# Kernel tuning notes

Hardware: AMD Instinct MI355X
Metric: run time of the kernel (lower is better)

Reference implementation:

```python
import jax, jax.numpy as jnp
import numpy as np

N_NODES = 100000
N_EDGES = 1600000
HID = 128
BOND = 16
BN_EPS = 1e-5


def setup_inputs() -> dict:
    key = jax.random.key(0)
    ks = jax.random.split(key, 12)
    sb = 1.0 / np.sqrt(BOND)
    sh = 1.0 / np.sqrt(HID)
    return {
        "features": jax.random.normal(ks[0], (N_NODES, HID), jnp.float32),
        "edge_feats": jax.random.normal(ks[1], (N_EDGES, BOND), jnp.float32),
        "src": jax.random.randint(ks[2], (N_EDGES,), 0, N_NODES, jnp.int32),
        "dst": jax.random.randint(ks[3], (N_EDGES,), 0, N_NODES, jnp.int32),
        "Wb": jax.random.uniform(ks[4], (HID, BOND), jnp.float32, -sb, sb),
        "bb": jax.random.uniform(ks[5], (HID,), jnp.float32, -sb, sb),
        "W1": jax.random.uniform(ks[6], (HID, HID), jnp.float32, -sh, sh),
        "b1": jax.random.uniform(ks[7], (HID,), jnp.float32, -sh, sh),
        "W2": jax.random.uniform(ks[8], (HID, HID), jnp.float32, -sh, sh),
        "b2": jax.random.uniform(ks[9], (HID,), jnp.float32, -sh, sh),
        "gamma1": jnp.ones((HID,), jnp.float32),
        "beta1": jnp.zeros((HID,), jnp.float32),
        "gamma2": jnp.ones((HID,), jnp.float32),
        "beta2": jnp.zeros((HID,), jnp.float32),
    }


def _batchnorm(x, gamma, beta):
    # BatchNorm1d in training mode: normalize with batch stats (biased var).
    mean = jnp.mean(x, axis=0)
    var = jnp.var(x, axis=0)
    return (x - mean) * jax.lax.rsqrt(var + BN_EPS) * gamma + beta


def reference(features, edge_feats, src, dst, Wb, bb, W1, b1, W2, b2,
              gamma1, beta1, gamma2, beta2):
    n = features.shape[0]
    # edge linear: [E, BOND] -> [E, HID]
    eh = edge_feats @ Wb.T + bb
    # mailbox sums: sum of src node features and edge messages per dst node
    h1 = jax.ops.segment_sum(features[src], dst, num_segments=n)  # [N, HID]
    h2 = jax.ops.segment_sum(eh, dst, num_segments=n)             # [N, HID]
    h = jax.nn.relu(_batchnorm(h1 @ W1.T + b1 + h2, gamma1, beta1))
    h = jax.nn.relu(_batchnorm(h @ W2.T + b2 + features, gamma2, beta2))
    return h
```

## Files before the change

kernel.cpp:

```cpp
#include <hip/hip_runtime.h>

#define NN 100000
#define NE 1600000
#define HID 128
#define KEXT 160
#define ROWB 320
#define BSH 9
#define BNODES 512
#define NB 196
#define P2B 256
#define EPB2 6250
#define T2 2048
#define BN_EPS 1e-5f

typedef __attribute__((ext_vector_type(8))) short bf16x8;
typedef __attribute__((ext_vector_type(4))) float f32x4;
typedef unsigned long long u64;

__device__ inline unsigned short f2bf(float x) {
  union { float f; unsigned u; } v; v.f = x;
  unsigned r = v.u + 0x7FFFu + ((v.u >> 16) & 1u);
  return (unsigned short)(r >> 16);
}
__device__ inline unsigned pk2(float a, float b) {
  return (unsigned)f2bf(a) | ((unsigned)f2bf(b) << 16);
}
__device__ inline float bflo(unsigned p) { return __uint_as_float(p << 16); }
__device__ inline float bfhi(unsigned p) { return __uint_as_float(p & 0xffff0000u); }

__device__ inline void gload_lds16(const void* g, void* l) {
  __builtin_amdgcn_global_load_lds((const __attribute__((address_space(1))) void*)g,
                                   (__attribute__((address_space(3))) void*)l, 16, 0, 0);
}

__global__ __launch_bounds__(256) void fbw_k(const float* __restrict__ f,
                                             unsigned* __restrict__ fb,
                                             const float* __restrict__ W1,
                                             const float* __restrict__ Wb,
                                             const float* __restrict__ bb,
                                             const float* __restrict__ b1,
                                             const float* __restrict__ W2,
                                             unsigned short* __restrict__ W1e,
                                             unsigned short* __restrict__ W2e) {
  if (blockIdx.x < 25000) {
    int i = blockIdx.x * 256 + threadIdx.x;
    float2 v = ((const float2*)f)[i];
    fb[i] = pk2(v.x, v.y);
  } else {
    int idx = (blockIdx.x - 25000) * 256 + threadIdx.x;
    if (idx < 128 * KEXT) {
      int c = idx / KEXT, k = idx - c * KEXT;
      float v1 = 0.f;
      if (k < 128) v1 = W1[c * HID + k];
      else if (k < 144) v1 = Wb[c * 16 + (k - 128)];
      else if (k == 144) v1 = bb[c];
      else if (k == 145) v1 = b1[c];
      W1e[idx] = f2bf(v1);
    }
    if (idx < 128 * 128) W2e[idx] = f2bf(W2[(idx >> 7) * HID + (idx & 127)]);
  }
}

__global__ __launch_bounds__(1024) void cnt_k(const int* __restrict__ dst,
                                              int* __restrict__ cnts_s) {
  __shared__ int bh[NB];
  int blk = blockIdx.x;
  int b0 = blk * EPB2, e1 = b0 + EPB2;
  for (int i = threadIdx.x; i < NB; i += 1024) bh[i] = 0;
  __syncthreads();
  for (int e = b0 + threadIdx.x; e < e1; e += 1024) atomicAdd(&bh[dst[e] >> BSH], 1);
  __syncthreads();
  for (int i = threadIdx.x; i < NB; i += 1024) cnts_s[i * P2B + blk] = bh[i];
}

__global__ __launch_bounds__(P2B) void cscan_k(int* __restrict__ cnts_s,
                                               int* __restrict__ cnts_e,
                                               int* __restrict__ bcnt_s,
                                               int* __restrict__ bcnt_e,
                                               int* __restrict__ bcnt_r) {
  __shared__ int s[P2B];
  int b = blockIdx.x, t = threadIdx.x;
  int x = cnts_s[b * P2B + t];
  int xs = (x + 7) & ~7;
  int xe = (x + 1) & ~1;
  s[t] = xs; __syncthreads();
  for (int off = 1; off < P2B; off <<= 1) {
    int v = (t >= off) ? s[t - off] : 0; __syncthreads();
    s[t] += v; __syncthreads();
  }
  cnts_s[b * P2B + t] = s[t] - xs;
  if (t == P2B - 1) bcnt_s[b] = s[t];
  __syncthreads();
  s[t] = xe; __syncthreads();
  for (int off = 1; off < P2B; off <<= 1) {
    int v = (t >= off) ? s[t - off] : 0; __syncthreads();
    s[t] += v; __syncthreads();
  }
  cnts_e[b * P2B + t] = s[t] - xe;
  if (t == P2B - 1) bcnt_e[b] = s[t];
  __syncthreads();
  s[t] = x; __syncthreads();
  for (int off = 1; off < P2B; off <<= 1) {
    int v = (t >= off) ? s[t - off] : 0; __syncthreads();
    s[t] += v; __syncthreads();
  }
  if (t == P2B - 1) bcnt_r[b] = s[t];
}

__global__ __launch_bounds__(256) void bscan_k(const int* __restrict__ bcnt_r,
                                               const int* __restrict__ bcnt_s,
                                               const int* __restrict__ bcnt_e,
                                               int* __restrict__ bbase_r,
                                               int* __restrict__ bbase_s,
                                               int* __restrict__ bbase_e,
                                               int* __restrict__ rs) {
  __shared__ int s[256];
  int t = threadIdx.x;
#pragma unroll
  for (int pass = 0; pass < 3; ++pass) {
    const int* in = (pass == 0) ? bcnt_r : (pass == 1) ? bcnt_s : bcnt_e;
    int* out = (pass == 0) ? bbase_r : (pass == 1) ? bbase_s : bbase_e;
    int x = (t < NB) ? in[t] : 0;
    s[t] = x; __syncthreads();
    for (int off = 1; off < 256; off <<= 1) {
      int v = (t >= off) ? s[t - off] : 0; __syncthreads();
      s[t] += v; __syncthreads();
    }
    if (t < NB) out[t] = s[t] - x;
    if (t == NB - 1) out[NB] = s[t];
    __syncthreads();
  }
  if (t == 0) rs[NN] = NE;
}

__global__ __launch_bounds__(1024) void part3_k(const int* __restrict__ src,
                                                const int* __restrict__ dst,
                                                const float* __restrict__ ef,
                                                const int* __restrict__ bbase_s,
                                                const int* __restrict__ bbase_e,
                                                const int* __restrict__ cnts_s,
                                                const int* __restrict__ cnts_e,
                                                u64* __restrict__ stg,
                                                float4* __restrict__ efb) {
  __shared__ int th[NB], ts[NB], cnt2[NB], run[NB], st_s[NB], st_e[NB];
  __shared__ int sscan[256];
  __shared__ unsigned spk[T2];
  __shared__ float4 eflds[T2 * 2];
  int blk = blockIdx.x, tid = threadIdx.x;
  int b0 = blk * EPB2, e1 = b0 + EPB2;
  for (int i = tid; i < NB; i += 1024) {
    run[i] = 0;
    st_s[i] = bbase_s[i] + cnts_s[i * P2B + blk];
    st_e[i] = bbase_e[i] + cnts_e[i * P2B + blk];
  }
  for (int t0 = b0; t0 < e1; t0 += T2) {
    int tc = min(T2, e1 - t0);
    for (int i = tid; i < NB; i += 1024) { th[i] = 0; cnt2[i] = 0; }
    __syncthreads();
    for (int le = tid; le < tc; le += 1024) {
      int e = t0 + le;
      atomicAdd(&th[dst[e] >> BSH], 1);
      const float4* efp = (const float4*)(ef + (size_t)e * 16);
      float4 e0 = efp[0], e1v = efp[1], e2 = efp[2], e3 = efp[3];
      float4 w0, w1;
      w0.x = __uint_as_float(pk2(e0.x, e0.y));  w0.y = __uint_as_float(pk2(e0.z, e0.w));
      w0.z = __uint_as_float(pk2(e1v.x, e1v.y)); w0.w = __uint_as_float(pk2(e1v.z, e1v.w));
      w1.x = __uint_as_float(pk2(e2.x, e2.y));  w1.y = __uint_as_float(pk2(e2.z, e2.w));
      w1.z = __uint_as_float(pk2(e3.x, e3.y));  w1.w = __uint_as_float(pk2(e3.z, e3.w));
      eflds[le * 2] = w0;
      eflds[le * 2 + 1] = w1;
    }
    __syncthreads();
    if (tid < 256) sscan[tid] = (tid < NB) ? th[tid] : 0;
    __syncthreads();
    for (int off = 1; off < 256; off <<= 1) {
      int v = 0;
      if (tid < 256 && tid >= off) v = sscan[tid - off];
      __syncthreads();
      if (tid < 256) sscan[tid] += v;
      __syncthreads();
    }
    if (tid < NB) ts[tid] = sscan[tid] - th[tid];
    __syncthreads();
    for (int le = tid; le < tc; le += 1024) {
      int b = dst[t0 + le] >> BSH;
      int slot = ts[b] + atomicAdd(&cnt2[b], 1);
      spk[slot] = ((unsigned)b << 11) | (unsigned)le;
    }
    __syncthreads();
    for (int s2 = tid; s2 < tc; s2 += 1024) {
      unsigned pk = spk[s2];
      int b = pk >> 11, le = pk & 2047;
      int e = t0 + le;
      int o = run[b] + (s2 - ts[b]);
      int gs = st_s[b] + o;
      int ge = st_e[b] + o;
      int d9 = dst[e] & (BNODES - 1);
      stg[gs] = (u64)(unsigned)src[e] | ((u64)(unsigned)d9 << 17) |
                (1ULL << 26) | ((u64)(unsigned)ge << 27);
      efb[(size_t)ge * 2] = eflds[le * 2];
      efb[(size_t)ge * 2 + 1] = eflds[le * 2 + 1];
    }
    __syncthreads();
    for (int i = tid; i < NB; i += 1024) run[i] += th[i];
    __syncthreads();
  }
  float4 z4 = make_float4(0.f, 0.f, 0.f, 0.f);
  for (int i = tid; i < NB; i += 1024) {
    int c = run[i];
    int cs = (c + 7) & ~7;
    for (int j = c; j < cs; ++j) stg[st_s[i] + j] = 0ULL;
    if (c & 1) {
      int ge = st_e[i] + c;
      efb[(size_t)ge * 2] = z4;
      efb[(size_t)ge * 2 + 1] = z4;
    }
  }
}

__global__ __launch_bounds__(512) void bsort_k(const u64* __restrict__ stg,
                                               const int* __restrict__ bbase_s,
                                               const int* __restrict__ bbase_r,
                                               int* __restrict__ rs,
                                               u64* __restrict__ fin) {
  __shared__ int h[BNODES], cur[BNODES], sc[BNODES];
  int b = blockIdx.x, n0 = b << BSH, tid = threadIdx.x;
  int s0p = bbase_s[b], e1p = bbase_s[b + 1];
  int s0r = bbase_r[b];
  h[tid] = 0;
  __syncthreads();
  for (int i = s0p + tid; i < e1p; i += 512) {
    u64 rec = stg[i];
    if ((rec >> 26) & 1) atomicAdd(&h[(int)(rec >> 17) & (BNODES - 1)], 1);
  }
  __syncthreads();
  sc[tid] = h[tid];
  __syncthreads();
  for (int off = 1; off < BNODES; off <<= 1) {
    int v = (tid >= off) ? sc[tid - off] : 0;
    __syncthreads();
    sc[tid] += v;
    __syncthreads();
  }
  {
    int excl = sc[tid] - h[tid];
    cur[tid] = s0r + excl;
    int n = n0 + tid;
    if (n < NN) rs[n] = s0r + excl;
  }
  __syncthreads();
  for (int i = s0p + tid; i < e1p; i += 512) {
    u64 rec = stg[i];
    if ((rec >> 26) & 1) {
      int d = (int)(rec >> 17) & (BNODES - 1);
      int p = atomicAdd(&cur[d], 1);
      fin[p] = (rec & 0x1FFFF) | (((rec >> 27) & 0x1FFFFF) << 17);
    }
  }
}

__global__ __launch_bounds__(256) void feg_k(const unsigned* __restrict__ fb,
                                             const int* __restrict__ rs,
                                             const u64* __restrict__ fin,
                                             const unsigned* __restrict__ efb,
                                             unsigned short* __restrict__ A1) {
  int bid = (int)(blockIdx.x & 7) * 3125 + (int)(blockIdx.x >> 3);
  int wid = threadIdx.x >> 6, lane = threadIdx.x & 63;
  int node = bid * 4 + wid;
  if (node >= NN) return;
  int start = rs[node], end = rs[node + 1];
  int j8 = lane & 7, es = lane >> 3;
  float ax0 = 0.f, ay0 = 0.f, ax1 = 0.f, ay1 = 0.f;
  float ax2 = 0.f, ay2 = 0.f, ax3 = 0.f, ay3 = 0.f;
  float ax4 = 0.f, ay4 = 0.f, ax5 = 0.f, ay5 = 0.f;
  float ax6 = 0.f, ay6 = 0.f, ax7 = 0.f, ay7 = 0.f;
  float efx = 0.f, efy = 0.f;
  int i = start;
  for (; i + 8 <= end; i += 8) {
    int sl = 0, el = 0;
    if (lane < 8) {
      u64 pk = fin[i + lane];
      sl = (int)(pk & 0x1FFFF);
      el = (int)((pk >> 17) & 0x1FFFFF);
    }
    int s0 = __shfl(sl, 0), s1 = __shfl(sl, 1), s2 = __shfl(sl, 2), s3 = __shfl(sl, 3);
    int s4 = __shfl(sl, 4), s5 = __shfl(sl, 5), s6 = __shfl(sl, 6), s7 = __shfl(sl, 7);
    int pes = __shfl(el, es);
    unsigned p0 = fb[s0 * 64 + lane];
    unsigned p1 = fb[s1 * 64 + lane];
    unsigned p2 = fb[s2 * 64 + lane];
    unsigned p3 = fb[s3 * 64 + lane];
    unsigned p4 = fb[s4 * 64 + lane];
    unsigned p5 = fb[s5 * 64 + lane];
    unsigned p6 = fb[s6 * 64 + lane];
    unsigned p7 = fb[s7 * 64 + lane];
    unsigned ev = efb[(size_t)pes * 8 + j8];
    ax0 += bflo(p0); ay0 += bfhi(p0);
    ax1 += bflo(p1); ay1 += bfhi(p1);
    ax2 += bflo(p2); ay2 += bfhi(p2);
    ax3 += bflo(p3); ay3 += bfhi(p3);
    ax4 += bflo(p4); ay4 += bfhi(p4);
    ax5 += bflo(p5); ay5 += bfhi(p5);
    ax6 += bflo(p6); ay6 += bfhi(p6);
    ax7 += bflo(p7); ay7 += bfhi(p7);
    efx += bflo(ev); efy += bfhi(ev);
  }
  for (; i < end; ++i) {
    int sl = 0, el = 0;
    if (lane == 0) {
      u64 pk = fin[i];
      sl = (int)(pk & 0x1FFFF);
      el = (int)((pk >> 17) & 0x1FFFFF);
    }
    int s0 = __shfl(sl, 0), e0 = __shfl(el, 0);
    unsigned p0 = fb[s0 * 64 + lane];
    ax0 += bflo(p0); ay0 += bfhi(p0);
    if (lane < 8) {
      unsigned ev = efb[(size_t)e0 * 8 + j8];
      efx += bflo(ev); efy += bfhi(ev);
    }
  }
  efx += __shfl_xor(efx, 8);  efy += __shfl_xor(efy, 8);
  efx += __shfl_xor(efx, 16); efy += __shfl_xor(efy, 16);
  efx += __shfl_xor(efx, 32); efy += __shfl_xor(efy, 32);
  float ax = ((ax0 + ax1) + (ax2 + ax3)) + ((ax4 + ax5) + (ax6 + ax7));
  float ay = ((ay0 + ay1) + (ay2 + ay3)) + ((ay4 + ay5) + (ay6 + ay7));
  char* rowp = (char*)A1 + (size_t)node * ROWB;
  *(unsigned*)(rowp + lane * 4) = pk2(ax, ay);
  if (lane < 8) {
    *(unsigned*)(rowp + 256 + 4 * j8) = pk2(efx, efy);
  } else if (lane < 16) {
    int j2 = lane - 8;
    *(unsigned*)(rowp + 288 + 4 * j2) =
        (j2 == 0) ? pk2((float)(end - start), 1.0f) : 0u;
  }
}

__global__ __launch_bounds__(256) void gemm1_k(
    const unsigned short* __restrict__ A, const unsigned short* __restrict__ W,
    unsigned short* __restrict__ outb, float* __restrict__ ssum, float* __restrict__ ssq) {
  __shared__ __align__(16) char sA[64 * ROWB];
  __shared__ __align__(16) char sW[128 * ROWB];
  const int tid = threadIdx.x;
  const int wid = tid >> 6, lane = tid & 63;
  const size_t r0 = (size_t)blockIdx.x * 64;

#pragma unroll
  for (int q = 0; q < 5; ++q) {
    int s = q * 256 + tid;
    int row = (s * 3277) >> 16;
    int c = s - row * 20;
    int csrc = (c < 16) ? (c ^ (row & 7)) : (16 + ((c - 16) ^ (row & 3)));
    gload_lds16((const char*)A + (r0 + row) * ROWB + csrc * 16,
                sA + (size_t)(q * 256 + wid * 64) * 16);
  }
#pragma unroll
  for (int q = 0; q < 10; ++q) {
    int s = q * 256 + tid;
    int row = (s * 3277) >> 16;
    int c = s - row * 20;
    int csrc = (c < 16) ? (c ^ (row & 7)) : (16 + ((c - 16) ^ (row & 3)));
    gload_lds16((const char*)W + (size_t)row * ROWB + csrc * 16,
                sW + (size_t)(q * 256 + wid * 64) * 16);
  }
  __syncthreads();

  const int l15 = lane & 15;
  const int kgr = lane >> 4;
  const int arow = wid * 16 + l15;
  bf16x8 afrag[5];
#pragma unroll
  for (int ks = 0; ks < 5; ++ks) {
    int creq = ks * 4 + kgr;
    int csw = (creq < 16) ? (creq ^ (arow & 7)) : (16 + ((creq - 16) ^ (arow & 3)));
    afrag[ks] = *(const bf16x8*)(sA + arow * ROWB + csw * 16);
  }
  f32x4 acc[8];
#pragma unroll
  for (int ct = 0; ct < 8; ++ct) acc[ct] = (f32x4){0.f, 0.f, 0.f, 0.f};
#pragma unroll
  for (int ct = 0; ct < 8; ++ct) {
    int brow = ct * 16 + l15;
#pragma unroll
    for (int ks = 0; ks < 5; ++ks) {
      int creq = ks * 4 + kgr;
      int csw = (creq < 16) ? (creq ^ (brow & 7)) : (16 + ((creq - 16) ^ (brow & 3)));
      bf16x8 bfrag = *(const bf16x8*)(sW + brow * ROWB + csw * 16);
      acc[ct] = __builtin_amdgcn_mfma_f32_16x16x32_bf16(afrag[ks], bfrag, acc[ct], 0, 0, 0);
    }
  }

  const size_t orow0 = r0 + wid * 16 + kgr * 4;
  float cs[8], cq[8];
#pragma unroll
  for (int ct = 0; ct < 8; ++ct) {
    int col = ct * 16 + l15;
    float s_ = 0.f, q_ = 0.f;
#pragma unroll
    for (int r = 0; r < 4; ++r) {
      size_t row = orow0 + r;
      if (row < NN) {
        float v = acc[ct][r];
        outb[row * HID + col] = f2bf(v);
        s_ += v; q_ += v * v;
      }
    }
    cs[ct] = s_; cq[ct] = q_;
  }
#pragma unroll
  for (int ct = 0; ct < 8; ++ct) {
    cs[ct] += __shfl_xor(cs[ct], 16); cs[ct] += __shfl_xor(cs[ct], 32);
    cq[ct] += __shfl_xor(cq[ct], 16); cq[ct] += __shfl_xor(cq[ct], 32);
  }
  __syncthreads();
  float* red = (float*)sA;
  if (lane < 16) {
#pragma unroll
    for (int ct = 0; ct < 8; ++ct) {
      red[wid * 256 + ct * 16 + l15] = cs[ct];
      red[wid * 256 + 128 + ct * 16 + l15] = cq[ct];
    }
  }
  __syncthreads();
  if (tid < 128) {
    float s_ = red[tid] + red[256 + tid] + red[512 + tid] + red[768 + tid];
    float q_ = red[128 + tid] + red[384 + tid] + red[640 + tid] + red[896 + tid];
    atomicAdd(&ssum[tid], s_);
    atomicAdd(&ssq[tid], q_);
  }
}

__global__ __launch_bounds__(256) void gemm2_k(
    const unsigned* __restrict__ t, const unsigned short* __restrict__ W,
    const float* __restrict__ ssum, const float* __restrict__ ssq,
    const float* __restrict__ gamma, const float* __restrict__ beta,
    const float* __restrict__ b2, const float* __restrict__ F,
    unsigned short* __restrict__ outb, float* __restrict__ ssum2,
    float* __restrict__ ssq2) {
  __shared__ __align__(16) char sA[64 * 256];
  __shared__ __align__(16) char sW[128 * 256];
  __shared__ float ssc[128], ssh[128];
  const int tid = threadIdx.x;
  const int wid = tid >> 6, lane = tid & 63;
  const size_t r0 = (size_t)blockIdx.x * 64;

  if (tid < 128) {
    const float invN = 1.f / (float)NN;
    float m = ssum[tid] * invN;
    float var = ssq[tid] * invN - m * m;
    float inv = rsqrtf(var + BN_EPS);
    float sc = gamma[tid] * inv;
    ssc[tid] = sc;
    ssh[tid] = beta[tid] - m * sc;
  }
#pragma unroll
  for (int q = 0; q < 8; ++q) {
    int s = q * 256 + tid;
    int row = s >> 4, c = s & 15;
    int csrc = c ^ (row & 7);
    gload_lds16((const char*)W + (size_t)row * 256 + csrc * 16,
                sW + (size_t)(q * 256 + wid * 64) * 16);
  }
  __syncthreads();

  {
    int sr = tid >> 2;
    int c0 = (tid & 3) * 4;
    size_t grow = r0 + sr;
    bool valid = grow < NN;
    const unsigned* trow = t + grow * 64;
#pragma unroll
    for (int cc = 0; cc < 4; ++cc) {
      int c = c0 + cc;
      unsigned o0 = 0, o1 = 0, o2 = 0, o3 = 0;
      if (valid) {
        unsigned p0 = trow[c * 4 + 0], p1 = trow[c * 4 + 1];
        unsigned p2 = trow[c * 4 + 2], p3 = trow[c * 4 + 3];
        int k = c * 8;
        o0 = pk2(fmaxf(0.f, fmaf(bflo(p0), ssc[k + 0], ssh[k + 0])),
                 fmaxf(0.f, fmaf(bfhi(p0), ssc[k + 1], ssh[k + 1])));
        o1 = pk2(fmaxf(0.f, fmaf(bflo(p1), ssc[k + 2], ssh[k + 2])),
                 fmaxf(0.f, fmaf(bfhi(p1), ssc[k + 3], ssh[k + 3])));
        o2 = pk2(fmaxf(0.f, fmaf(bflo(p2), ssc[k + 4], ssh[k + 4])),
                 fmaxf(0.f, fmaf(bfhi(p2), ssc[k + 5], ssh[k + 5])));
        o3 = pk2(fmaxf(0.f, fmaf(bflo(p3), ssc[k + 6], ssh[k + 6])),
                 fmaxf(0.f, fmaf(bfhi(p3), ssc[k + 7], ssh[k + 7])));
      }
      int csw = c ^ (sr & 7);
      uint4 w4; w4.x = o0; w4.y = o1; w4.z = o2; w4.w = o3;
      *(uint4*)(sA + sr * 256 + csw * 16) = w4;
    }
  }
  __syncthreads();

  const int l15 = lane & 15;
  const int kgr = lane >> 4;
  const int arow = wid * 16 + l15;
  bf16x8 afrag[4];
#pragma unroll
  for (int ks = 0; ks < 4; ++ks) {
    int creq = ks * 4 + kgr;
    int csw = creq ^ (arow & 7);
    afrag[ks] = *(const bf16x8*)(sA + arow * 256 + csw * 16);
  }
  f32x4 acc[8];
#pragma unroll
  for (int ct = 0; ct < 8; ++ct) acc[ct] = (f32x4){0.f, 0.f, 0.f, 0.f};
#pragma unroll
  for (int ct = 0; ct < 8; ++ct) {
    int brow = ct * 16 + l15;
#pragma unroll
    for (int ks = 0; ks < 4; ++ks) {
      int creq = ks * 4 + kgr;
      int csw = creq ^ (brow & 7);
      bf16x8 bfrag = *(const bf16x8*)(sW + brow * 256 + csw * 16);
      acc[ct] = __builtin_amdgcn_mfma_f32_16x16x32_bf16(afrag[ks], bfrag, acc[ct], 0, 0, 0);
    }
  }

  const size_t orow0 = r0 + wid * 16 + kgr * 4;
  float cs[8], cq[8];
#pragma unroll
  for (int ct = 0; ct < 8; ++ct) {
    int col = ct * 16 + l15;
    float b2v = b2[col];
    float s_ = 0.f, q_ = 0.f;
#pragma unroll
    for (int r = 0; r < 4; ++r) {
      size_t row = orow0 + r;
      if (row < NN) {
        float v = acc[ct][r] + b2v + F[row * HID + col];
        outb[row * HID + col] = f2bf(v);
        s_ += v; q_ += v * v;
      }
    }
    cs[ct] = s_; cq[ct] = q_;
  }
#pragma unroll
  for (int ct = 0; ct < 8; ++ct) {
    cs[ct] += __shfl_xor(cs[ct], 16); cs[ct] += __shfl_xor(cs[ct], 32);
    cq[ct] += __shfl_xor(cq[ct], 16); cq[ct] += __shfl_xor(cq[ct], 32);
  }
  __syncthreads();
  float* red = (float*)sA;
  if (lane < 16) {
#pragma unroll
    for (int ct = 0; ct < 8; ++ct) {
      red[wid * 256 + ct * 16 + l15] = cs[ct];
      red[wid * 256 + 128 + ct * 16 + l15] = cq[ct];
    }
  }
  __syncthreads();
  if (tid < 128) {
    float s_ = red[tid] + red[256 + tid] + red[512 + tid] + red[768 + tid];
    float q_ = red[128 + tid] + red[384 + tid] + red[640 + tid] + red[896 + tid];
    atomicAdd(&ssum2[tid], s_);
    atomicAdd(&ssq2[tid], q_);
  }
}

__global__ __launch_bounds__(256) void bn_final_k(const unsigned* __restrict__ t,
                                                  const float* __restrict__ ssum,
                                                  const float* __restrict__ ssq,
                                                  const float* __restrict__ gamma,
                                                  const float* __restrict__ beta,
                                                  float* __restrict__ o) {
  __shared__ float ssc[128], ssh[128];
  int tid = threadIdx.x;
  if (tid < 128) {
    const float invN = 1.f / (float)NN;
    float m = ssum[tid] * invN;
    float var = ssq[tid] * invN - m * m;
    float inv = rsqrtf(var + BN_EPS);
    float sc = gamma[tid] * inv;
    ssc[tid] = sc;
    ssh[tid] = beta[tid] - m * sc;
  }
  __syncthreads();
  int i = blockIdx.x * 256 + tid;
  if (i >= NN * 64) return;
  unsigned p = t[i];
  int c = (i & 63) * 2;
  float2 v;
  v.x = fmaxf(0.f, fmaf(bflo(p), ssc[c], ssh[c]));
  v.y = fmaxf(0.f, fmaf(bfhi(p), ssc[c + 1], ssh[c + 1]));
  ((float2*)o)[i] = v;
}

extern "C" void kernel_launch(void* const* d_in, const int* in_sizes, int n_in,
                              void* d_out, int out_size, void* d_ws, size_t ws_size,
                              hipStream_t stream) {
  (void)in_sizes; (void)n_in; (void)out_size; (void)ws_size;
  const float* features   = (const float*)d_in[0];
  const float* edge_feats = (const float*)d_in[1];
  const int*   src        = (const int*)d_in[2];
  const int*   dst        = (const int*)d_in[3];
  const float* Wb         = (const float*)d_in[4];
  const float* bb         = (const float*)d_in[5];
  const float* W1         = (const float*)d_in[6];
  const float* b1         = (const float*)d_in[7];
  const float* W2         = (const float*)d_in[8];
  const float* b2         = (const float*)d_in[9];
  const float* gamma1     = (const float*)d_in[10];
  const float* beta1      = (const float*)d_in[11];
  const float* gamma2     = (const float*)d_in[12];
  const float* beta2      = (const float*)d_in[13];
  float* outp = (float*)d_out;

  char* wsb = (char*)d_ws;
  size_t off = 0;
  auto alloc = [&](size_t nbytes) -> void* {
    off = (off + 255) & ~(size_t)255;
    void* p = wsb + off;
    off += nbytes;
    return p;
  };
  int* row_start = (int*)alloc((size_t)(NN + 1) * 4);
  int* bcnt_r    = (int*)alloc(NB * 4);
  int* bcnt_s    = (int*)alloc(NB * 4);
  int* bcnt_e    = (int*)alloc(NB * 4);
  int* bbase_r   = (int*)alloc((NB + 1) * 4);
  int* bbase_s   = (int*)alloc((NB + 1) * 4);
  int* bbase_e   = (int*)alloc((NB + 1) * 4);
  int* cnts_s    = (int*)alloc((size_t)NB * P2B * 4);
  int* cnts_e    = (int*)alloc((size_t)NB * P2B * 4);
  float* stats   = (float*)alloc(512 * 4);
  unsigned* featb = (unsigned*)alloc((size_t)NN * 64 * 4);
  unsigned short* A1e = (unsigned short*)alloc((size_t)100032 * ROWB);
  unsigned short* W1e = (unsigned short*)alloc(128 * KEXT * 2);
  unsigned short* W2e = (unsigned short*)alloc(128 * 128 * 2);
  u64* stg       = (u64*)alloc((size_t)(NE + 7 * NB * P2B + 64) * 8);
  u64* fin       = (u64*)alloc((size_t)NE * 8);
  float4* efb    = (float4*)alloc((size_t)(NE + NB * P2B + 64) * 32);
  unsigned short* tbuf = (unsigned short*)featb;

  hipMemsetAsync(stats, 0, 512 * 4, stream);
  hipMemsetAsync((char*)A1e + (size_t)NN * ROWB, 0, 32 * ROWB, stream);

  fbw_k<<<25080, 256, 0, stream>>>(features, featb, W1, Wb, bb, b1, W2, W1e, W2e);
  cnt_k<<<P2B, 1024, 0, stream>>>(dst, cnts_s);
  cscan_k<<<NB, P2B, 0, stream>>>(cnts_s, cnts_e, bcnt_s, bcnt_e, bcnt_r);
  bscan_k<<<1, 256, 0, stream>>>(bcnt_r, bcnt_s, bcnt_e, bbase_r, bbase_s, bbase_e,
                                 row_start);
  part3_k<<<P2B, 1024, 0, stream>>>(src, dst, edge_feats, bbase_s, bbase_e,
                                    cnts_s, cnts_e, stg, efb);
  bsort_k<<<NB, 512, 0, stream>>>(stg, bbase_s, bbase_r, row_start, fin);
  feg_k<<<25000, 256, 0, stream>>>(featb, row_start, fin, (const unsigned*)efb, A1e);

  gemm1_k<<<1563, 256, 0, stream>>>(A1e, W1e, tbuf, stats, stats + 128);
  gemm2_k<<<1563, 256, 0, stream>>>((const unsigned*)tbuf, W2e, stats, stats + 128,
                                    gamma1, beta1, b2, features, tbuf,
                                    stats + 256, stats + 384);
  bn_final_k<<<25000, 256, 0, stream>>>((const unsigned*)tbuf, stats + 256, stats + 384,
                                        gamma2, beta2, outp);
}
```

Baseline: 327.6 us.

## Fold dst histogram into prep kernel and pre-reduce edge features in bucket sort

The dst bucket-count kernel is merged into the feature/weight conversion launch as extra blocks, which removes one launch. The separate edge-feature staging offsets (cnts_e/bbase_e scans) are dropped. Edge features now share the sort staging index, and records shrink from 64-bit to 32-bit. bsort_k sorts records in LDS and sums each node's bf16 edge features into an efsum buffer, so feg_k no longer gathers per-edge features. The cost is a serial per-thread loop in bsort_k over each node's edges, plus an LDS capacity assumption (SCAP) on bucket size.

```diff
diff --git a/kernel.cpp b/kernel.cpp
--- a/kernel.cpp
+++ b/kernel.cpp
@@ -11,11 +11,11 @@
 #define P2B 256
 #define EPB2 6250
 #define T2 2048
+#define SCAP 10240
 #define BN_EPS 1e-5f
 
 typedef __attribute__((ext_vector_type(8))) short bf16x8;
 typedef __attribute__((ext_vector_type(4))) float f32x4;
-typedef unsigned long long u64;
 
 __device__ inline unsigned short f2bf(float x) {
   union { float f; unsigned u; } v; v.f = x;
@@ -41,12 +41,15 @@
                                              const float* __restrict__ b1,
                                              const float* __restrict__ W2,
                                              unsigned short* __restrict__ W1e,
-                                             unsigned short* __restrict__ W2e) {
+                                             unsigned short* __restrict__ W2e,
+                                             const int* __restrict__ dst,
+                                             int* __restrict__ cnts_s) {
+  __shared__ int bh[NB];
   if (blockIdx.x < 25000) {
     int i = blockIdx.x * 256 + threadIdx.x;
     float2 v = ((const float2*)f)[i];
     fb[i] = pk2(v.x, v.y);
-  } else {
+  } else if (blockIdx.x < 25080) {
     int idx = (blockIdx.x - 25000) * 256 + threadIdx.x;
     if (idx < 128 * KEXT) {
       int c = idx / KEXT, k = idx - c * KEXT;
@@ -58,31 +61,24 @@
       W1e[idx] = f2bf(v1);
     }
     if (idx < 128 * 128) W2e[idx] = f2bf(W2[(idx >> 7) * HID + (idx & 127)]);
-  }
-}
-
-__global__ __launch_bounds__(1024) void cnt_k(const int* __restrict__ dst,
-                                              int* __restrict__ cnts_s) {
-  __shared__ int bh[NB];
-  int blk = blockIdx.x;
-  int b0 = blk * EPB2, e1 = b0 + EPB2;
-  for (int i = threadIdx.x; i < NB; i += 1024) bh[i] = 0;
-  __syncthreads();
-  for (int e = b0 + threadIdx.x; e < e1; e += 1024) atomicAdd(&bh[dst[e] >> BSH], 1);
-  __syncthreads();
-  for (int i = threadIdx.x; i < NB; i += 1024) cnts_s[i * P2B + blk] = bh[i];
+  } else {
+    int blk = blockIdx.x - 25080;
+    int b0 = blk * EPB2, e1 = b0 + EPB2;
+    for (int i = threadIdx.x; i < NB; i += 256) bh[i] = 0;
+    __syncthreads();
+    for (int e = b0 + threadIdx.x; e < e1; e += 256) atomicAdd(&bh[dst[e] >> BSH], 1);
+    __syncthreads();
+    for (int i = threadIdx.x; i < NB; i += 256) cnts_s[i * P2B + blk] = bh[i];
+  }
 }
 
 __global__ __launch_bounds__(P2B) void cscan_k(int* __restrict__ cnts_s,
-                                               int* __restrict__ cnts_e,
                                                int* __restrict__ bcnt_s,
-                                               int* __restrict__ bcnt_e,
                                                int* __restrict__ bcnt_r) {
   __shared__ int s[P2B];
   int b = blockIdx.x, t = threadIdx.x;
   int x = cnts_s[b * P2B + t];
   int xs = (x + 7) & ~7;
-  int xe = (x + 1) & ~1;
   s[t] = xs; __syncthreads();
   for (int off = 1; off < P2B; off <<= 1) {
     int v = (t >= off) ? s[t - off] : 0; __syncthreads();
@@ -91,14 +87,6 @@
   cnts_s[b * P2B + t] = s[t] - xs;
   if (t == P2B - 1) bcnt_s[b] = s[t];
   __syncthreads();
-  s[t] = xe; __syncthreads();
-  for (int off = 1; off < P2B; off <<= 1) {
-    int v = (t >= off) ? s[t - off] : 0; __syncthreads();
-    s[t] += v; __syncthreads();
-  }
-  cnts_e[b * P2B + t] = s[t] - xe;
-  if (t == P2B - 1) bcnt_e[b] = s[t];
-  __syncthreads();
   s[t] = x; __syncthreads();
   for (int off = 1; off < P2B; off <<= 1) {
     int v = (t >= off) ? s[t - off] : 0; __syncthreads();
@@ -109,17 +97,15 @@
 
 __global__ __launch_bounds__(256) void bscan_k(const int* __restrict__ bcnt_r,
                                                const int* __restrict__ bcnt_s,
-                                               const int* __restrict__ bcnt_e,
                                                int* __restrict__ bbase_r,
                                                int* __restrict__ bbase_s,
-                                               int* __restrict__ bbase_e,
                                                int* __restrict__ rs) {
   __shared__ int s[256];
   int t = threadIdx.x;
 #pragma unroll
-  for (int pass = 0; pass < 3; ++pass) {
-    const int* in = (pass == 0) ? bcnt_r : (pass == 1) ? bcnt_s : bcnt_e;
-    int* out = (pass == 0) ? bbase_r : (pass == 1) ? bbase_s : bbase_e;
+  for (int pass = 0; pass < 2; ++pass) {
+    const int* in = (pass == 0) ? bcnt_r : bcnt_s;
+    int* out = (pass == 0) ? bbase_r : bbase_s;
     int x = (t < NB) ? in[t] : 0;
     s[t] = x; __syncthreads();
     for (int off = 1; off < 256; off <<= 1) {
@@ -137,12 +123,10 @@
                                                 const int* __restrict__ dst,
                                                 const float* __restrict__ ef,
                                                 const int* __restrict__ bbase_s,
-                                                const int* __restrict__ bbase_e,
                                                 const int* __restrict__ cnts_s,
-                                                const int* __restrict__ cnts_e,
-                                                u64* __restrict__ stg,
+                                                unsigned* __restrict__ stg,
                                                 float4* __restrict__ efb) {
-  __shared__ int th[NB], ts[NB], cnt2[NB], run[NB], st_s[NB], st_e[NB];
+  __shared__ int th[NB], ts[NB], cnt2[NB], run[NB], st_s[NB];
   __shared__ int sscan[256];
   __shared__ unsigned spk[T2];
   __shared__ float4 eflds[T2 * 2];
@@ -151,7 +135,6 @@
   for (int i = tid; i < NB; i += 1024) {
     run[i] = 0;
     st_s[i] = bbase_s[i] + cnts_s[i * P2B + blk];
-    st_e[i] = bbase_e[i] + cnts_e[i * P2B + blk];
   }
   for (int t0 = b0; t0 < e1; t0 += T2) {
     int tc = min(T2, e1 - t0);
@@ -192,46 +175,41 @@
       unsigned pk = spk[s2];
       int b = pk >> 11, le = pk & 2047;
       int e = t0 + le;
-      int o = run[b] + (s2 - ts[b]);
-      int gs = st_s[b] + o;
-      int ge = st_e[b] + o;
+      int gs = st_s[b] + run[b] + (s2 - ts[b]);
       int d9 = dst[e] & (BNODES - 1);
-      stg[gs] = (u64)(unsigned)src[e] | ((u64)(unsigned)d9 << 17) |
-                (1ULL << 26) | ((u64)(unsigned)ge << 27);
-      efb[(size_t)ge * 2] = eflds[le * 2];
-      efb[(size_t)ge * 2 + 1] = eflds[le * 2 + 1];
+      stg[gs] = (unsigned)src[e] | ((unsigned)d9 << 17) | (1u << 26);
+      efb[(size_t)gs * 2] = eflds[le * 2];
+      efb[(size_t)gs * 2 + 1] = eflds[le * 2 + 1];
     }
     __syncthreads();
     for (int i = tid; i < NB; i += 1024) run[i] += th[i];
     __syncthreads();
   }
-  float4 z4 = make_float4(0.f, 0.f, 0.f, 0.f);
   for (int i = tid; i < NB; i += 1024) {
     int c = run[i];
     int cs = (c + 7) & ~7;
-    for (int j = c; j < cs; ++j) stg[st_s[i] + j] = 0ULL;
-    if (c & 1) {
-      int ge = st_e[i] + c;
-      efb[(size_t)ge * 2] = z4;
-      efb[(size_t)ge * 2 + 1] = z4;
-    }
-  }
-}
-
-__global__ __launch_bounds__(512) void bsort_k(const u64* __restrict__ stg,
+    for (int j = c; j < cs; ++j) stg[st_s[i] + j] = 0u;
+  }
+}
+
+__global__ __launch_bounds__(512) void bsort_k(const unsigned* __restrict__ stg,
                                                const int* __restrict__ bbase_s,
                                                const int* __restrict__ bbase_r,
+                                               const unsigned* __restrict__ efbu,
                                                int* __restrict__ rs,
-                                               u64* __restrict__ fin) {
-  __shared__ int h[BNODES], cur[BNODES], sc[BNODES];
+                                               unsigned* __restrict__ fin,
+                                               unsigned* __restrict__ efsum) {
+  __shared__ int h[BNODES], sc[BNODES], cur[BNODES];
+  __shared__ int tot;
+  __shared__ unsigned slds[SCAP];
   int b = blockIdx.x, n0 = b << BSH, tid = threadIdx.x;
   int s0p = bbase_s[b], e1p = bbase_s[b + 1];
   int s0r = bbase_r[b];
   h[tid] = 0;
   __syncthreads();
   for (int i = s0p + tid; i < e1p; i += 512) {
-    u64 rec = stg[i];
-    if ((rec >> 26) & 1) atomicAdd(&h[(int)(rec >> 17) & (BNODES - 1)], 1);
+    unsigned rec = stg[i];
+    if (rec >> 26) atomicAdd(&h[(rec >> 17) & (BNODES - 1)], 1);
   }
   __syncthreads();
   sc[tid] = h[tid];
@@ -242,50 +220,63 @@
     sc[tid] += v;
     __syncthreads();
   }
-  {
-    int excl = sc[tid] - h[tid];
-    cur[tid] = s0r + excl;
-    int n = n0 + tid;
-    if (n < NN) rs[n] = s0r + excl;
-  }
+  int excl = sc[tid] - h[tid];
+  cur[tid] = excl;
+  int n = n0 + tid;
+  if (n < NN) rs[n] = s0r + excl;
+  if (tid == BNODES - 1) tot = sc[tid];
   __syncthreads();
   for (int i = s0p + tid; i < e1p; i += 512) {
-    u64 rec = stg[i];
-    if ((rec >> 26) & 1) {
-      int d = (int)(rec >> 17) & (BNODES - 1);
+    unsigned rec = stg[i];
+    if (rec >> 26) {
+      int d = (rec >> 17) & (BNODES - 1);
       int p = atomicAdd(&cur[d], 1);
-      fin[p] = (rec & 0x1FFFF) | (((rec >> 27) & 0x1FFFFF) << 17);
-    }
+      slds[p] = (rec & 0x1FFFF) | ((unsigned)(i - s0p) << 17);
+    }
+  }
+  __syncthreads();
+  int T = tot;
+  for (int j = tid; j < T; j += 512) fin[s0r + j] = slds[j] & 0x1FFFF;
+  if (n < NN) {
+    float a[16];
+#pragma unroll
+    for (int k = 0; k < 16; ++k) a[k] = 0.f;
+    for (int j = excl; j < sc[tid]; ++j) {
+      unsigned rec = slds[j];
+      const unsigned* ep = efbu + ((size_t)s0p + (rec >> 17)) * 8;
+#pragma unroll
+      for (int k = 0; k < 8; ++k) {
+        unsigned u = ep[k];
+        a[2 * k] += bflo(u);
+        a[2 * k + 1] += bfhi(u);
+      }
+    }
+    unsigned* op = efsum + (size_t)n * 8;
+#pragma unroll
+    for (int k = 0; k < 8; ++k) op[k] = pk2(a[2 * k], a[2 * k + 1]);
   }
 }
 
 __global__ __launch_bounds__(256) void feg_k(const unsigned* __restrict__ fb,
                                              const int* __restrict__ rs,
-                                             const u64* __restrict__ fin,
-                                             const unsigned* __restrict__ efb,
+                                             const unsigned* __restrict__ fin,
+                                             const unsigned* __restrict__ efsum,
                                              unsigned short* __restrict__ A1) {
   int bid = (int)(blockIdx.x & 7) * 3125 + (int)(blockIdx.x >> 3);
   int wid = threadIdx.x >> 6, lane = threadIdx.x & 63;
   int node = bid * 4 + wid;
   if (node >= NN) return;
   int start = rs[node], end = rs[node + 1];
-  int j8 = lane & 7, es = lane >> 3;
   float ax0 = 0.f, ay0 = 0.f, ax1 = 0.f, ay1 = 0.f;
   float ax2 = 0.f, ay2 = 0.f, ax3 = 0.f, ay3 = 0.f;
   float ax4 = 0.f, ay4 = 0.f, ax5 = 0.f, ay5 = 0.f;
   float ax6 = 0.f, ay6 = 0.f, ax7 = 0.f, ay7 = 0.f;
-  float efx = 0.f, efy = 0.f;
   int i = start;
   for (; i + 8 <= end; i += 8) {
-    int sl = 0, el = 0;
-    if (lane < 8) {
-      u64 pk = fin[i + lane];
-      sl = (int)(pk & 0x1FFFF);
-      el = (int)((pk >> 17) & 0x1FFFFF);
-    }
+    int sl = 0;
+    if (lane < 8) sl = (int)fin[i + lane];
     int s0 = __shfl(sl, 0), s1 = __shfl(sl, 1), s2 = __shfl(sl, 2), s3 = __shfl(sl, 3);
     int s4 = __shfl(sl, 4), s5 = __shfl(sl, 5), s6 = __shfl(sl, 6), s7 = __shfl(sl, 7);
-    int pes = __shfl(el, es);
     unsigned p0 = fb[s0 * 64 + lane];
     unsigned p1 = fb[s1 * 64 + lane];
     unsigned p2 = fb[s2 * 64 + lane];
@@ -294,7 +285,6 @@
     unsigned p5 = fb[s5 * 64 + lane];
     unsigned p6 = fb[s6 * 64 + lane];
     unsigned p7 = fb[s7 * 64 + lane];
-    unsigned ev = efb[(size_t)pes * 8 + j8];
     ax0 += bflo(p0); ay0 += bfhi(p0);
     ax1 += bflo(p1); ay1 += bfhi(p1);
     ax2 += bflo(p2); ay2 += bfhi(p2);
@@ -303,32 +293,20 @@
     ax5 += bflo(p5); ay5 += bfhi(p5);
     ax6 += bflo(p6); ay6 += bfhi(p6);
     ax7 += bflo(p7); ay7 += bfhi(p7);
-    efx += bflo(ev); efy += bfhi(ev);
   }
   for (; i < end; ++i) {
-    int sl = 0, el = 0;
-    if (lane == 0) {
-      u64 pk = fin[i];
-      sl = (int)(pk & 0x1FFFF);
-      el = (int)((pk >> 17) & 0x1FFFFF);
-    }
-    int s0 = __shfl(sl, 0), e0 = __shfl(el, 0);
+    int sl = 0;
+    if (lane == 0) sl = (int)fin[i];
+    int s0 = __shfl(sl, 0);
     unsigned p0 = fb[s0 * 64 + lane];
     ax0 += bflo(p0); ay0 += bfhi(p0);
-    if (lane < 8) {
-      unsigned ev = efb[(size_t)e0 * 8 + j8];
-      efx += bflo(ev); efy += bfhi(ev);
-    }
-  }
-  efx += __shfl_xor(efx, 8);  efy += __shfl_xor(efy, 8);
-  efx += __shfl_xor(efx, 16); efy += __shfl_xor(efy, 16);
-  efx += __shfl_xor(efx, 32); efy += __shfl_xor(efy, 32);
+  }
   float ax = ((ax0 + ax1) + (ax2 + ax3)) + ((ax4 + ax5) + (ax6 + ax7));
   float ay = ((ay0 + ay1) + (ay2 + ay3)) + ((ay4 + ay5) + (ay6 + ay7));
   char* rowp = (char*)A1 + (size_t)node * ROWB;
   *(unsigned*)(rowp + lane * 4) = pk2(ax, ay);
   if (lane < 8) {
-    *(unsigned*)(rowp + 256 + 4 * j8) = pk2(efx, efy);
+    *(unsigned*)(rowp + 256 + 4 * lane) = efsum[(size_t)node * 8 + lane];
   } else if (lane < 16) {
     int j2 = lane - 8;
     *(unsigned*)(rowp + 288 + 4 * j2) =
@@ -615,37 +593,35 @@
     off += nbytes;
     return p;
   };
+  const size_t STGN = (size_t)NE + 7 * NB * P2B + 64;
   int* row_start = (int*)alloc((size_t)(NN + 1) * 4);
   int* bcnt_r    = (int*)alloc(NB * 4);
   int* bcnt_s    = (int*)alloc(NB * 4);
-  int* bcnt_e    = (int*)alloc(NB * 4);
   int* bbase_r   = (int*)alloc((NB + 1) * 4);
   int* bbase_s   = (int*)alloc((NB + 1) * 4);
-  int* bbase_e   = (int*)alloc((NB + 1) * 4);
   int* cnts_s    = (int*)alloc((size_t)NB * P2B * 4);
-  int* cnts_e    = (int*)alloc((size_t)NB * P2B * 4);
   float* stats   = (float*)alloc(512 * 4);
   unsigned* featb = (unsigned*)alloc((size_t)NN * 64 * 4);
   unsigned short* A1e = (unsigned short*)alloc((size_t)100032 * ROWB);
   unsigned short* W1e = (unsigned short*)alloc(128 * KEXT * 2);
   unsigned short* W2e = (unsigned short*)alloc(128 * 128 * 2);
-  u64* stg       = (u64*)alloc((size_t)(NE + 7 * NB * P2B + 64) * 8);
-  u64* fin       = (u64*)alloc((size_t)NE * 8);
-  float4* efb    = (float4*)alloc((size_t)(NE + NB * P2B + 64) * 32);
+  unsigned* stg  = (unsigned*)alloc(STGN * 4);
+  unsigned* fin  = (unsigned*)alloc((size_t)NE * 4);
+  float4* efb    = (float4*)alloc(STGN * 32);
+  unsigned* efsum = (unsigned*)alloc((size_t)NN * 32);
   unsigned short* tbuf = (unsigned short*)featb;
 
   hipMemsetAsync(stats, 0, 512 * 4, stream);
   hipMemsetAsync((char*)A1e + (size_t)NN * ROWB, 0, 32 * ROWB, stream);
 
-  fbw_k<<<25080, 256, 0, stream>>>(features, featb, W1, Wb, bb, b1, W2, W1e, W2e);
-  cnt_k<<<P2B, 1024, 0, stream>>>(dst, cnts_s);
-  cscan_k<<<NB, P2B, 0, stream>>>(cnts_s, cnts_e, bcnt_s, bcnt_e, bcnt_r);
-  bscan_k<<<1, 256, 0, stream>>>(bcnt_r, bcnt_s, bcnt_e, bbase_r, bbase_s, bbase_e,
-                                 row_start);
-  part3_k<<<P2B, 1024, 0, stream>>>(src, dst, edge_feats, bbase_s, bbase_e,
-                                    cnts_s, cnts_e, stg, efb);
-  bsort_k<<<NB, 512, 0, stream>>>(stg, bbase_s, bbase_r, row_start, fin);
-  feg_k<<<25000, 256, 0, stream>>>(featb, row_start, fin, (const unsigned*)efb, A1e);
+  fbw_k<<<25336, 256, 0, stream>>>(features, featb, W1, Wb, bb, b1, W2, W1e, W2e,
+                                   dst, cnts_s);
+  cscan_k<<<NB, P2B, 0, stream>>>(cnts_s, bcnt_s, bcnt_r);
+  bscan_k<<<1, 256, 0, stream>>>(bcnt_r, bcnt_s, bbase_r, bbase_s, row_start);
+  part3_k<<<P2B, 1024, 0, stream>>>(src, dst, edge_feats, bbase_s, cnts_s, stg, efb);
+  bsort_k<<<NB, 512, 0, stream>>>(stg, bbase_s, bbase_r, (const unsigned*)efb,
+                                  row_start, fin, efsum);
+  feg_k<<<25000, 256, 0, stream>>>(featb, row_start, fin, efsum, A1e);
 
   gemm1_k<<<1563, 256, 0, stream>>>(A1e, W1e, tbuf, stats, stats + 128);
   gemm2_k<<<1563, 256, 0, stream>>>((const unsigned*)tbuf, W2e, stats, stats + 128,
```

Result: no change. 333.0 us (+1.7%).
